# Optimization experiments

Measured on AMD Instinct MI355X. Metric: run time of the kernel, lower is better.

The kernel has to match this reference:

```python
import jax, jax.numpy as jnp
import numpy as np

EPS = 1e-5  # torch nn.LayerNorm default


def layer_norm(x, g, b):
    mu = jnp.mean(x, axis=-1, keepdims=True)
    var = jnp.mean(jnp.square(x - mu), axis=-1, keepdims=True)
    return (x - mu) * jax.lax.rsqrt(var + EPS) * g + b


def run_dir(g_ih_seq, w_hh, g_hh, b_hh, g_ho, b_ho, reverse):
    """Run one LayerNormLSTMCell direction over precomputed LN(x @ W_ih^T).
    g_ih_seq: [S, B, 4H]. Returns final hidden [B, H]."""
    S, B, G = g_ih_seq.shape
    H = G // 4

    def step(carry, gih_t):
        h, c = carry
        gates = gih_t + layer_norm(h @ w_hh.T, g_hh, b_hh)  # [B, 4H]
        i, f, o = jnp.split(jax.nn.sigmoid(gates[:, : 3 * H]), 3, axis=1)
        g = jnp.tanh(gates[:, 3 * H :])
        c = f * c + i * g
        h = o * jnp.tanh(layer_norm(c, g_ho, b_ho))
        return (h, c), None

    z = jnp.zeros((B, H), g_ih_seq.dtype)
    (hT, _), _ = jax.lax.scan(step, (z, z), g_ih_seq, reverse=reverse)
    return hT


def lnlstm(x, w_ih0, w_hh0, ln_ih0_g, ln_ih0_b, ln_hh0_g, ln_hh0_b, ln_ho0_g,
           ln_ho0_b, w_ih1, w_hh1, ln_ih1_g, ln_ih1_b, ln_hh1_g, ln_hh1_b,
           ln_ho1_g, ln_ho1_b):
    # x: [B, S, E] -> permute(1,0,2)
    x_seq = jnp.transpose(x, (1, 0, 2))  # [S, B, E]
    S, B, _ = x_seq.shape

    # ---- layer 0 (time-varying input) ----
    g0f = layer_norm(jnp.einsum('sbe,ge->sbg', x_seq, w_ih0[0]), ln_ih0_g[0], ln_ih0_b[0])
    hf = run_dir(g0f, w_hh0[0], ln_hh0_g[0], ln_hh0_b[0], ln_ho0_g[0], ln_ho0_b[0], False)
    g0b = layer_norm(jnp.einsum('sbe,ge->sbg', x_seq, w_ih0[1]), ln_ih0_g[1], ln_ih0_b[1])
    hb = run_dir(g0b, w_hh0[1], ln_hh0_g[1], ln_hh0_b[1], ln_ho0_g[1], ln_ho0_b[1], True)

    # Due to the `[[None]*N]*seq_len` aliasing bug in the original torch code,
    # the next layer's input is the SAME vector at every timestep:
    xc = jnp.concatenate([hf, hb], axis=1)  # [B, 2H]

    # ---- layer 1 (constant input; LN(x@W_ih^T) computed once, broadcast over time) ----
    g1f = layer_norm(xc @ w_ih1[0].T, ln_ih1_g[0], ln_ih1_b[0])
    hf1 = run_dir(jnp.broadcast_to(g1f, (S,) + g1f.shape), w_hh1[0],
                  ln_hh1_g[0], ln_hh1_b[0], ln_ho1_g[0], ln_ho1_b[0], False)
    g1b = layer_norm(xc @ w_ih1[1].T, ln_ih1_g[1], ln_ih1_b[1])
    hb1 = run_dir(jnp.broadcast_to(g1b, (S,) + g1b.shape), w_hh1[1],
                  ln_hh1_g[1], ln_hh1_b[1], ln_ho1_g[1], ln_ho1_b[1], True)

    # y = max over time of identical vectors == the vector itself
    return jnp.concatenate([hf1, hb1], axis=1)  # [B, 2H]


def setup_inputs() -> dict:
    key = jax.random.key(0)
    ks = jax.random.split(key, 20)
    B, S, E, H = 64, 48, 512, 512
    f = jnp.float32
    n = jax.random.normal
    u = jax.random.uniform
    return {
        'x': n(ks[0], (B, S, E), f),
        'text_length': jax.random.randint(ks[1], (B,), 1, S),
        'w_ih0': n(ks[2], (2, 4 * H, E), f) * 0.05,
        'w_hh0': n(ks[3], (2, 4 * H, H), f) * 0.05,
        'ln_ih0_g': u(ks[4], (2, 4 * H), f, 0.5, 1.5),
        'ln_ih0_b': n(ks[5], (2, 4 * H), f) * 0.02,
        'ln_hh0_g': u(ks[6], (2, 4 * H), f, 0.5, 1.5),
        'ln_hh0_b': n(ks[7], (2, 4 * H), f) * 0.02,
        'ln_ho0_g': u(ks[8], (2, H), f, 0.5, 1.5),
        'ln_ho0_b': n(ks[9], (2, H), f) * 0.02,
        'w_ih1': n(ks[10], (2, 4 * H, 2 * H), f) * 0.05,
        'w_hh1': n(ks[11], (2, 4 * H, H), f) * 0.05,
        'ln_ih1_g': u(ks[12], (2, 4 * H), f, 0.5, 1.5),
        'ln_ih1_b': n(ks[13], (2, 4 * H), f) * 0.02,
        'ln_hh1_g': u(ks[14], (2, 4 * H), f, 0.5, 1.5),
        'ln_hh1_b': n(ks[15], (2, 4 * H), f) * 0.02,
        'ln_ho1_g': u(ks[16], (2, H), f, 0.5, 1.5),
        'ln_ho1_b': n(ks[17], (2, H), f) * 0.02,
    }


def reference(x, text_length, w_ih0, w_hh0, ln_ih0_g, ln_ih0_b, ln_hh0_g,
              ln_hh0_b, ln_ho0_g, ln_ho0_b, w_ih1, w_hh1, ln_ih1_g, ln_ih1_b,
              ln_hh1_g, ln_hh1_b, ln_ho1_g, ln_ho1_b):
    # text_length is accepted but unused by the original forward
    return lnlstm(x, w_ih0, w_hh0, ln_ih0_g, ln_ih0_b, ln_hh0_g, ln_hh0_b,
                  ln_ho0_g, ln_ho0_b, w_ih1, w_hh1, ln_ih1_g, ln_ih1_b,
                  ln_hh1_g, ln_hh1_b, ln_ho1_g, ln_ho1_b)
```

## Files before the change

### kernel.cpp

```cpp
#include <hip/hip_runtime.h>
#include <math.h>

#define HH 512
#define BB 64
#define SS 48
#define EE 512
#define G4 2048
#define EPSF 1e-5f
#define AGENT __HIP_MEMORY_SCOPE_AGENT

__device__ __forceinline__ float aload(const float* p) {
  return __hip_atomic_load(p, __ATOMIC_RELAXED, AGENT);
}
__device__ __forceinline__ void astore(float* p, float v) {
  __hip_atomic_store(p, v, __ATOMIC_RELAXED, AGENT);
}

__device__ __forceinline__ float fsigmoid(float x) {
  float t = __builtin_amdgcn_exp2f(x * -1.44269504088896f);
  return __builtin_amdgcn_rcpf(1.f + t);
}
__device__ __forceinline__ float ftanh(float x) {
  x = fminf(fmaxf(x, -10.f), 10.f);
  float t = __builtin_amdgcn_exp2f(x * 2.88539008177793f);
  return (t - 1.f) * __builtin_amdgcn_rcpf(t + 1.f);
}

__device__ __forceinline__ void gsync(int* c, int target) {
  __builtin_amdgcn_s_waitcnt(0);
  __syncthreads();
  if (threadIdx.x == 0) {
    __hip_atomic_fetch_add(c, 1, __ATOMIC_RELEASE, AGENT);
    int spins = 0;
    while (__hip_atomic_load(c, __ATOMIC_RELAXED, AGENT) < target) {
      __builtin_amdgcn_s_sleep(2);
      if (++spins > (1 << 21)) break;
    }
    (void)__hip_atomic_load(c, __ATOMIC_ACQUIRE, AGENT);
  }
  __syncthreads();
}

__global__ __launch_bounds__(256)
void gemm_ih0(const float* __restrict__ x, const float* __restrict__ w_ih0,
              float* __restrict__ G0) {
  __shared__ float As[16][65];
  __shared__ float Bs[16][65];
  const int m0 = blockIdx.y * 64;
  const int d  = m0 / (BB * SS);
  const float* Wm = w_ih0 + (size_t)d * G4 * EE;
  const int bn = blockIdx.x * 64;
  const int tid = threadIdx.x;
  const int lrow = tid >> 2;
  const int lkk  = (tid & 3) << 2;
  const int tx = tid & 15;
  const int ty = tid >> 4;
  int m  = m0 + lrow;
  int r  = m - d * (BB * SS);
  int b  = r / SS;
  int tl = r - b * SS;
  int s  = d ? (SS - 1 - tl) : tl;
  const float* arow = x + ((size_t)b * SS + s) * EE;

  float acc[4][4] = {};
  for (int k0 = 0; k0 < EE; k0 += 16) {
    float4 av = *(const float4*)(arow + k0 + lkk);
    float4 bv = *(const float4*)(Wm + (size_t)(bn + lrow) * EE + k0 + lkk);
    As[lkk+0][lrow] = av.x; As[lkk+1][lrow] = av.y; As[lkk+2][lrow] = av.z; As[lkk+3][lrow] = av.w;
    Bs[lkk+0][lrow] = bv.x; Bs[lkk+1][lrow] = bv.y; Bs[lkk+2][lrow] = bv.z; Bs[lkk+3][lrow] = bv.w;
    __syncthreads();
    #pragma unroll
    for (int k = 0; k < 16; ++k) {
      float a[4], bbv[4];
      #pragma unroll
      for (int i = 0; i < 4; ++i) a[i] = As[k][ty*4+i];
      #pragma unroll
      for (int j = 0; j < 4; ++j) bbv[j] = Bs[k][tx*4+j];
      #pragma unroll
      for (int i = 0; i < 4; ++i)
        #pragma unroll
        for (int j = 0; j < 4; ++j) acc[i][j] += a[i]*bbv[j];
    }
    __syncthreads();
  }
  for (int i = 0; i < 4; ++i)
    for (int j = 0; j < 4; ++j)
      G0[(size_t)(m0 + ty*4 + i) * G4 + bn + tx*4 + j] = acc[i][j];
}

__global__ __launch_bounds__(256)
void ln_rows(float* __restrict__ X, const float* __restrict__ gamma,
             const float* __restrict__ beta, int rows_per_d) {
  __shared__ float red[8];
  const int row = blockIdx.x;
  const int d = row / rows_per_d;
  float* xr = X + (size_t)row * G4;
  const float* gg = gamma + (size_t)d * G4;
  const float* bb = beta  + (size_t)d * G4;
  float s = 0.f, q = 0.f;
  float v[8];
  #pragma unroll
  for (int it = 0; it < 8; ++it) {
    float xv = xr[threadIdx.x + it*256];
    v[it] = xv; s += xv; q += xv*xv;
  }
  #pragma unroll
  for (int off = 32; off > 0; off >>= 1) { s += __shfl_down(s, off); q += __shfl_down(q, off); }
  int lane = threadIdx.x & 63, wid = threadIdx.x >> 6;
  if (lane == 0) { red[wid] = s; red[4+wid] = q; }
  __syncthreads();
  float ts = red[0]+red[1]+red[2]+red[3];
  float tq = red[4]+red[5]+red[6]+red[7];
  float mu = ts * (1.f/G4);
  float rstd = rsqrtf(tq*(1.f/G4) - mu*mu + EPSF);
  #pragma unroll
  for (int it = 0; it < 8; ++it) {
    int jc = threadIdx.x + it*256;
    xr[jc] = (v[it]-mu)*rstd*gg[jc] + bb[jc];
  }
}

__global__ __launch_bounds__(1024, 4)
void persist7(const float* __restrict__ whh, const float* __restrict__ Gbuf,
              long g_row_stride, long g_t_stride,
              const float* __restrict__ lnhg, const float* __restrict__ lnhb,
              const float* __restrict__ lnog, const float* __restrict__ lnob,
              float* cbuf, float* obuf, float* Rpart, float* Cpart,
              int* flagsA, int* flagsB,
              float* fout, int nsteps,
              int mode1, const float* __restrict__ w_ih1,
              const float* __restrict__ xcb, float* g1pre,
              const float* __restrict__ ln_g1, const float* __restrict__ ln_b1,
              int* cnt_pre) {
  __shared__ float hlds[16][1024];
  __shared__ float part[16][8][64];
  __shared__ float redR[16][64];
  __shared__ float bcR[16][2];
  __shared__ float bcC[16][2];
  __shared__ float sred[32];

  const int bb = blockIdx.x;
  const int tid = threadIdx.x;

  if (mode1) {
    const int dp = bb & 1, nbp = bb >> 1;
    const int pb = tid >> 4, ns = tid & 15;
    const int col = nbp*16 + ns;
    const float* xrow = xcb + (size_t)pb * 1024;
    const float* wv_ = w_ih1 + ((size_t)dp*G4 + col) * 1024;
    float a = 0.f;
    for (int k = 0; k < 1024; k += 4) {
      float4 xv = *(const float4*)(xrow + k);
      float4 wv4 = *(const float4*)(wv_ + k);
      a += xv.x*wv4.x + xv.y*wv4.y + xv.z*wv4.z + xv.w*wv4.w;
    }
    astore(g1pre + ((size_t)dp*BB + pb) * G4 + col, a);
    gsync(cnt_pre + 0, 256);
    if (bb < 128) {
      const int ld = bb >> 6;
      float* xr = g1pre + (size_t)bb * G4;
      const float* gg = ln_g1 + (size_t)ld * G4;
      const float* be = ln_b1 + (size_t)ld * G4;
      float v0 = aload(xr + tid), v1 = aload(xr + tid + 1024);
      float s = v0 + v1, q = v0*v0 + v1*v1;
      #pragma unroll
      for (int off = 32; off > 0; off >>= 1) { s += __shfl_down(s, off); q += __shfl_down(q, off); }
      const int wv2 = tid >> 6;
      if ((tid & 63) == 0) { sred[wv2] = s; sred[16+wv2] = q; }
      __syncthreads();
      float ts = 0.f, tq = 0.f;
      #pragma unroll
      for (int i = 0; i < 16; ++i) { ts += sred[i]; tq += sred[16+i]; }
      float mu = ts * (1.f/G4);
      float rstd = rsqrtf(tq*(1.f/G4) - mu*mu + EPSF);
      astore(xr + tid,        (v0-mu)*rstd*gg[tid]      + be[tid]);
      astore(xr + tid + 1024, (v1-mu)*rstd*gg[tid+1024] + be[tid+1024]);
    }
    gsync(cnt_pre + 16, 256);
  }

  const int g  = bb & 7;
  const int d  = g >> 2;
  const int bq = g & 3;
  const int jb = bb >> 3;
  const int rowbase = d*BB + bq*16;
  const int ke = tid >> 6, nl = tid & 63;
  const int ncol = jb*16 + ((nl>>4) << 9) + (nl & 15);
  int* fA = flagsA + g*1024;
  int* fB = flagsB + g*1024;

  float wreg[32];
  {
    const float* wp = whh + ((size_t)d*G4 + ncol)*HH + (size_t)ke*32;
    #pragma unroll
    for (int i = 0; i < 32; ++i) wreg[i] = wp[i];
  }

  const int bl = tid >> 4, jl = tid & 15;
  const int rowc = rowbase + bl;
  const int jc = jb*16 + jl;
  const int scol = tid & 511, srh = tid >> 9;
  const float ogv = lnog[(size_t)d*HH + scol];
  const float obv = lnob[(size_t)d*HH + scol];
  const int row16 = tid >> 5, j32 = tid & 31;
  const int inv_g = (g_t_stride == 0);

  float hg0=0,hg1=0,hg2=0,hg3=0, hb0=0,hb1=0,hb2=0,hb3=0;
  float cg0=0,cg1=0,cg2=0,cg3=0;
  if (tid < 256) {
    const float* lnhg_d = lnhg + (size_t)d*G4;
    const float* lnhb_d = lnhb + (size_t)d*G4;
    hg0 = lnhg_d[jc];        hb0 = lnhb_d[jc];
    hg1 = lnhg_d[HH+jc];     hb1 = lnhb_d[HH+jc];
    hg2 = lnhg_d[2*HH+jc];   hb2 = lnhb_d[2*HH+jc];
    hg3 = lnhg_d[3*HH+jc];   hb3 = lnhb_d[3*HH+jc];
    if (inv_g) {
      const float* gr = Gbuf + (size_t)rowc * g_row_stride;
      cg0 = gr[jc]; cg1 = gr[HH+jc]; cg2 = gr[2*HH+jc]; cg3 = gr[3*HH+jc];
    }
  }
  float creg = 0.f;

  for (int t = 0; t < nsteps; ++t) {
    float cv[8], ovv[8];
    #pragma unroll
    for (int i = 0; i < 8; ++i) {
      int row = i*2 + srh;
      cv[i]  = aload(cbuf + (size_t)(rowbase + row)*512 + scol);
      ovv[i] = aload(obuf + (size_t)(rowbase + row)*512 + scol);
    }
    if (tid < 512) {
      float s = aload(Cpart + ((size_t)(rowbase+row16)*32 + j32)*2 + 0);
      float q = aload(Cpart + ((size_t)(rowbase+row16)*32 + j32)*2 + 1);
      #pragma unroll
      for (int off = 16; off > 0; off >>= 1) { s += __shfl_down(s, off, 32); q += __shfl_down(q, off, 32); }
      if (j32 == 0) {
        float mu = s * (1.f/HH);
        bcC[row16][0] = mu;
        bcC[row16][1] = rsqrtf(q*(1.f/HH) - mu*mu + EPSF);
      }
    }
    __syncthreads();
    #pragma unroll
    for (int i = 0; i < 8; ++i) {
      int row = i*2 + srh;
      hlds[row][scol] = ovv[i] * ftanh((cv[i] - bcC[row][0]) * bcC[row][1] * ogv + obv);
    }
    __syncthreads();

    #pragma unroll
    for (int half = 0; half < 2; ++half) {
      #pragma unroll
      for (int b = 0; b < 8; ++b) {
        const float* hp = &hlds[half*8 + b][ke*32];
        float acc = 0.f;
        #pragma unroll
        for (int i4 = 0; i4 < 8; ++i4) {
          float4 h4 = *(const float4*)(hp + 4*i4);
          acc += h4.x*wreg[4*i4+0] + h4.y*wreg[4*i4+1]
               + h4.z*wreg[4*i4+2] + h4.w*wreg[4*i4+3];
        }
        part[ke][b][nl] = acc;
      }
      __syncthreads();
      if (tid < 512) {
        int b = tid >> 6, n2 = tid & 63;
        float r = 0.f;
        #pragma unroll
        for (int k16 = 0; k16 < 16; ++k16) r += part[k16][b][n2];
        redR[half*8 + b][n2] = r;
      }
      __syncthreads();
    }
    if (tid < 512) {
      float v1 = redR[row16][j32], v2 = redR[row16][j32+32];
      float s = v1 + v2, q = v1*v1 + v2*v2;
      #pragma unroll
      for (int off = 16; off > 0; off >>= 1) { s += __shfl_down(s, off, 32); q += __shfl_down(q, off, 32); }
      if (j32 == 0) {
        astore(Rpart + ((size_t)(rowbase+row16)*32 + jb)*2 + 0, s);
        astore(Rpart + ((size_t)(rowbase+row16)*32 + jb)*2 + 1, q);
      }
    }
    float pg0 = cg0, pg1 = cg1, pg2 = cg2, pg3 = cg3;
    if (tid < 256 && !inv_g) {
      const float* gr = Gbuf + (size_t)rowc * g_row_stride + (size_t)t * g_t_stride;
      pg0 = gr[jc]; pg1 = gr[HH+jc]; pg2 = gr[2*HH+jc]; pg3 = gr[3*HH+jc];
    }
    __syncthreads();
    if (tid == 0) __hip_atomic_store(fA + jb*32, t + 1, __ATOMIC_RELAXED, AGENT);
    if (tid < 32) {
      int spins = 0;
      for (;;) {
        int v = __hip_atomic_load(fA + tid*32, __ATOMIC_RELAXED, AGENT);
        #pragma unroll
        for (int off = 16; off > 0; off >>= 1) v = min(v, __shfl_down(v, off, 32));
        v = __shfl(v, 0, 32);
        if (v >= t + 1) break;
        __builtin_amdgcn_s_sleep(1);
        if (++spins > (1 << 22)) break;
      }
    }
    __syncthreads();

    if (tid < 512) {
      float s = aload(Rpart + ((size_t)(rowbase+row16)*32 + j32)*2 + 0);
      float q = aload(Rpart + ((size_t)(rowbase+row16)*32 + j32)*2 + 1);
      #pragma unroll
      for (int off = 16; off > 0; off >>= 1) { s += __shfl_down(s, off, 32); q += __shfl_down(q, off, 32); }
      if (j32 == 0) {
        float mu = s * (1.f/G4);
        bcR[row16][0] = mu;
        bcR[row16][1] = rsqrtf(q*(1.f/G4) - mu*mu + EPSF);
      }
    }
    __syncthreads();

    if (tid < 256) {
      float mu = bcR[bl][0], rstd = bcR[bl][1];
      float gi = pg0 + (redR[bl][jl]    - mu)*rstd*hg0 + hb0;
      float gf = pg1 + (redR[bl][16+jl] - mu)*rstd*hg1 + hb1;
      float go = pg2 + (redR[bl][32+jl] - mu)*rstd*hg2 + hb2;
      float gt = pg3 + (redR[bl][48+jl] - mu)*rstd*hg3 + hb3;
      float iv = fsigmoid(gi), fv = fsigmoid(gf);
      float ov = fsigmoid(go), gv = ftanh(gt);
      creg = fv*creg + iv*gv;
      float cs = creg, cq = creg*creg;
      #pragma unroll
      for (int off = 8; off > 0; off >>= 1) { cs += __shfl_down(cs, off, 16); cq += __shfl_down(cq, off, 16); }
      if (jl == 0) {
        astore(Cpart + ((size_t)rowc*32 + jb)*2 + 0, cs);
        astore(Cpart + ((size_t)rowc*32 + jb)*2 + 1, cq);
      }
      astore(cbuf + (size_t)rowc*512 + jc, creg);
      astore(obuf + (size_t)rowc*512 + jc, ov);
    }
    __syncthreads();
    if (tid == 0) __hip_atomic_store(fB + jb*32, t + 1, __ATOMIC_RELAXED, AGENT);
    if (tid < 32) {
      int spins = 0;
      for (;;) {
        int v = __hip_atomic_load(fB + tid*32, __ATOMIC_RELAXED, AGENT);
        #pragma unroll
        for (int off = 16; off > 0; off >>= 1) v = min(v, __shfl_down(v, off, 32));
        v = __shfl(v, 0, 32);
        if (v >= t + 1) break;
        __builtin_amdgcn_s_sleep(1);
        if (++spins > (1 << 22)) break;
      }
    }
    __syncthreads();
  }

  {
    float cv[8], ovv[8];
    #pragma unroll
    for (int i = 0; i < 8; ++i) {
      int row = i*2 + srh;
      cv[i]  = aload(cbuf + (size_t)(rowbase + row)*512 + scol);
      ovv[i] = aload(obuf + (size_t)(rowbase + row)*512 + scol);
    }
    if (tid < 512) {
      float s = aload(Cpart + ((size_t)(rowbase+row16)*32 + j32)*2 + 0);
      float q = aload(Cpart + ((size_t)(rowbase+row16)*32 + j32)*2 + 1);
      #pragma unroll
      for (int off = 16; off > 0; off >>= 1) { s += __shfl_down(s, off, 32); q += __shfl_down(q, off, 32); }
      if (j32 == 0) {
        float mu = s * (1.f/HH);
        bcC[row16][0] = mu;
        bcC[row16][1] = rsqrtf(q*(1.f/HH) - mu*mu + EPSF);
      }
    }
    __syncthreads();
    if (jb == 0) {
      #pragma unroll
      for (int i = 0; i < 8; ++i) {
        int row = i*2 + srh;
        float h = ovv[i] * ftanh((cv[i] - bcC[row][0]) * bcC[row][1] * ogv + obv);
        fout[(size_t)(bq*16 + row) * 1024 + (size_t)d*512 + scol] = h;
      }
    }
  }
}

extern "C" void kernel_launch(void* const* d_in, const int* in_sizes, int n_in,
                              void* d_out, int out_size, void* d_ws, size_t ws_size,
                              hipStream_t stream) {
  const float* x        = (const float*)d_in[0];
  const float* w_ih0    = (const float*)d_in[2];
  const float* w_hh0    = (const float*)d_in[3];
  const float* ln_ih0_g = (const float*)d_in[4];
  const float* ln_ih0_b = (const float*)d_in[5];
  const float* ln_hh0_g = (const float*)d_in[6];
  const float* ln_hh0_b = (const float*)d_in[7];
  const float* ln_ho0_g = (const float*)d_in[8];
  const float* ln_ho0_b = (const float*)d_in[9];
  const float* w_ih1    = (const float*)d_in[10];
  const float* w_hh1    = (const float*)d_in[11];
  const float* ln_ih1_g = (const float*)d_in[12];
  const float* ln_ih1_b = (const float*)d_in[13];
  const float* ln_hh1_g = (const float*)d_in[14];
  const float* ln_hh1_b = (const float*)d_in[15];
  const float* ln_ho1_g = (const float*)d_in[16];
  const float* ln_ho1_b = (const float*)d_in[17];
  float* out = (float*)d_out;

  float* G0    = (float*)d_ws;
  float* g1pre = G0 + (size_t)2*BB*SS*G4;
  float* xcb   = g1pre + (size_t)2*BB*G4;
  float* Rpart = xcb + (size_t)BB*1024;
  float* Cpart = Rpart + (size_t)128*32*2;
  float* cbuf  = Cpart + (size_t)128*32*2;
  float* obuf  = cbuf + (size_t)128*512;
  int*   ints  = (int*)(obuf + (size_t)128*512);
  int*   fA0     = ints;
  int*   fB0     = ints + 8192;
  int*   fA1     = ints + 16384;
  int*   fB1     = ints + 24576;
  int*   cnt_pre = ints + 32768;

  hipMemsetAsync(Cpart, 0, ((size_t)128*32*2 + 2*(size_t)128*512)*sizeof(float)
                           + 32832*sizeof(int), stream);

  hipLaunchKernelGGL(gemm_ih0, dim3(G4/64, (2*BB*SS)/64), dim3(256), 0, stream,
      x, w_ih0, G0);
  hipLaunchKernelGGL(ln_rows, dim3(2*BB*SS), dim3(256), 0, stream,
      G0, ln_ih0_g, ln_ih0_b, BB*SS);

  hipLaunchKernelGGL(persist7, dim3(256), dim3(1024), 0, stream,
      w_hh0, G0, (long)SS*G4, (long)G4,
      ln_hh0_g, ln_hh0_b, ln_ho0_g, ln_ho0_b,
      cbuf, obuf, Rpart, Cpart, fA0, fB0, xcb, SS,
      0, (const float*)nullptr, (const float*)nullptr, (float*)nullptr,
      (const float*)nullptr, (const float*)nullptr, (int*)nullptr);

  hipMemsetAsync(Cpart, 0, ((size_t)128*32*2 + 2*(size_t)128*512)*sizeof(float), stream);

  hipLaunchKernelGGL(persist7, dim3(256), dim3(1024), 0, stream,
      w_hh1, g1pre, (long)G4, 0L,
      ln_hh1_g, ln_hh1_b, ln_ho1_g, ln_ho1_b,
      cbuf, obuf, Rpart, Cpart, fA1, fB1, out, SS,
      1, w_ih1, xcb, g1pre, ln_ih1_g, ln_ih1_b, cnt_pre);
}
```

Measured before the change: 1.752 ms.

## Compute recurrent LayerNorm statistics from h via precomputed Gram matrix W^T W

```diff
diff --git a/kernel.cpp b/kernel.cpp
--- a/kernel.cpp
+++ b/kernel.cpp
@@ -89,6 +89,54 @@
 }
 
 __global__ __launch_bounds__(256)
+void wtw(const float* __restrict__ w0, const float* __restrict__ w1,
+         float* __restrict__ M0, float* __restrict__ M1,
+         float* __restrict__ ws0, float* __restrict__ ws1) {
+  __shared__ float As[16][65];
+  __shared__ float Bs[16][65];
+  const int z = blockIdx.z;
+  const float* W = (z < 2 ? w0 : w1) + (size_t)(z & 1) * G4 * HH;
+  float* Mout  = (z < 2 ? M0 : M1) + (size_t)(z & 1) * HH * HH;
+  float* wsout = (z < 2 ? ws0 : ws1) + (size_t)(z & 1) * HH;
+  const int k1b = blockIdx.y * 64;
+  const int k2b = blockIdx.x * 64;
+  const int tid = threadIdx.x;
+  const int jj = tid >> 4;
+  const int c4 = (tid & 15) << 2;
+  const int tx = tid & 15, ty = tid >> 4;
+
+  float acc[4][4] = {};
+  float wsacc[4] = {0.f, 0.f, 0.f, 0.f};
+  for (int j0 = 0; j0 < G4; j0 += 16) {
+    float4 av = *(const float4*)(W + (size_t)(j0 + jj)*HH + k1b + c4);
+    float4 bv = *(const float4*)(W + (size_t)(j0 + jj)*HH + k2b + c4);
+    As[jj][c4+0]=av.x; As[jj][c4+1]=av.y; As[jj][c4+2]=av.z; As[jj][c4+3]=av.w;
+    Bs[jj][c4+0]=bv.x; Bs[jj][c4+1]=bv.y; Bs[jj][c4+2]=bv.z; Bs[jj][c4+3]=bv.w;
+    __syncthreads();
+    #pragma unroll
+    for (int k = 0; k < 16; ++k) {
+      float a[4], b[4];
+      #pragma unroll
+      for (int i = 0; i < 4; ++i) a[i] = As[k][ty*4+i];
+      #pragma unroll
+      for (int j = 0; j < 4; ++j) b[j] = Bs[k][tx*4+j];
+      #pragma unroll
+      for (int i = 0; i < 4; ++i) {
+        wsacc[i] += a[i];
+        #pragma unroll
+        for (int j = 0; j < 4; ++j) acc[i][j] += a[i]*b[j];
+      }
+    }
+    __syncthreads();
+  }
+  for (int i = 0; i < 4; ++i)
+    for (int j = 0; j < 4; ++j)
+      Mout[(size_t)(k1b + ty*4 + i)*HH + k2b + tx*4 + j] = acc[i][j];
+  if (blockIdx.x == 0 && tx == 0)
+    for (int i = 0; i < 4; ++i) wsout[k1b + ty*4 + i] = wsacc[i];
+}
+
+__global__ __launch_bounds__(256)
 void ln_rows(float* __restrict__ X, const float* __restrict__ gamma,
              const float* __restrict__ beta, int rows_per_d) {
   __shared__ float red[8];
@@ -131,13 +179,16 @@
               int mode1, const float* __restrict__ w_ih1,
               const float* __restrict__ xcb, float* g1pre,
               const float* __restrict__ ln_g1, const float* __restrict__ ln_b1,
-              int* cnt_pre) {
+              int* cnt_pre,
+              const float* __restrict__ Mmat, const float* __restrict__ wsum) {
   __shared__ float hlds[16][1024];
   __shared__ float part[16][8][64];
+  __shared__ float Mlds[16][512];
   __shared__ float redR[16][64];
   __shared__ float bcR[16][2];
   __shared__ float bcC[16][2];
   __shared__ float sred[32];
+  __shared__ float wsls[16];
 
   const int bb = blockIdx.x;
   const int tid = threadIdx.x;
@@ -196,6 +247,14 @@
     for (int i = 0; i < 32; ++i) wreg[i] = wp[i];
   }
 
+  {
+    float* mf = &Mlds[0][0];
+    const float* msrc = Mmat + (size_t)d*HH*HH + (size_t)(jb*16)*HH;
+    #pragma unroll
+    for (int u = 0; u < 8; ++u) mf[u*1024 + tid] = msrc[(size_t)u*1024 + tid];
+    if (tid < 16) wsls[tid] = wsum[(size_t)d*HH + jb*16 + tid];
+  }
+
   const int bl = tid >> 4, jl = tid & 15;
   const int rowc = rowbase + bl;
   const int jc = jb*16 + jl;
@@ -204,6 +263,7 @@
   const float obv = lnob[(size_t)d*HH + scol];
   const int row16 = tid >> 5, j32 = tid & 31;
   const int inv_g = (g_t_stride == 0);
+  const int kbase = jb*16;
 
   float hg0=0,hg1=0,hg2=0,hg3=0, hb0=0,hb1=0,hb2=0,hb3=0;
   float cg0=0,cg1=0,cg2=0,cg3=0;
@@ -248,6 +308,34 @@
     }
     __syncthreads();
 
+    if (tid < 512) {
+      const int r = row16;
+      float hreg[16];
+      #pragma unroll
+      for (int k1 = 0; k1 < 16; ++k1) hreg[k1] = hlds[r][kbase + k1];
+      float t_s = 0.f;
+      #pragma unroll
+      for (int k1 = 0; k1 < 16; ++k1) t_s += hreg[k1] * wsls[k1];
+      float t_q = 0.f;
+      #pragma unroll
+      for (int it = 0; it < 16; ++it) {
+        int k2 = j32 + 32*it;
+        float h2 = hlds[r][k2];
+        float dcol = 0.f;
+        #pragma unroll
+        for (int k1 = 0; k1 < 16; ++k1) dcol += Mlds[k1][k2] * hreg[k1];
+        t_q += h2 * dcol;
+      }
+      #pragma unroll
+      for (int off = 16; off > 0; off >>= 1) t_q += __shfl_down(t_q, off, 32);
+      if (j32 == 0) {
+        astore(Rpart + ((size_t)(rowbase+r)*32 + jb)*2 + 0, t_s);
+        astore(Rpart + ((size_t)(rowbase+r)*32 + jb)*2 + 1, t_q);
+      }
+    }
+    __syncthreads();
+    if (tid == 0) __hip_atomic_store(fA + jb*32, t + 1, __ATOMIC_RELAXED, AGENT);
+
     #pragma unroll
     for (int half = 0; half < 2; ++half) {
       #pragma unroll
@@ -272,23 +360,11 @@
       }
       __syncthreads();
     }
-    if (tid < 512) {
-      float v1 = redR[row16][j32], v2 = redR[row16][j32+32];
-      float s = v1 + v2, q = v1*v1 + v2*v2;
-      #pragma unroll
-      for (int off = 16; off > 0; off >>= 1) { s += __shfl_down(s, off, 32); q += __shfl_down(q, off, 32); }
-      if (j32 == 0) {
-        astore(Rpart + ((size_t)(rowbase+row16)*32 + jb)*2 + 0, s);
-        astore(Rpart + ((size_t)(rowbase+row16)*32 + jb)*2 + 1, q);
-      }
-    }
     float pg0 = cg0, pg1 = cg1, pg2 = cg2, pg3 = cg3;
     if (tid < 256 && !inv_g) {
       const float* gr = Gbuf + (size_t)rowc * g_row_stride + (size_t)t * g_t_stride;
       pg0 = gr[jc]; pg1 = gr[HH+jc]; pg2 = gr[2*HH+jc]; pg3 = gr[3*HH+jc];
     }
-    __syncthreads();
-    if (tid == 0) __hip_atomic_store(fA + jb*32, t + 1, __ATOMIC_RELAXED, AGENT);
     if (tid < 32) {
       int spins = 0;
       for (;;) {
@@ -409,7 +485,11 @@
   float* g1pre = G0 + (size_t)2*BB*SS*G4;
   float* xcb   = g1pre + (size_t)2*BB*G4;
   float* Rpart = xcb + (size_t)BB*1024;
-  float* Cpart = Rpart + (size_t)128*32*2;
+  float* M0    = Rpart + (size_t)128*32*2;
+  float* M1    = M0 + (size_t)2*HH*HH;
+  float* ws0   = M1 + (size_t)2*HH*HH;
+  float* ws1   = ws0 + (size_t)2*HH;
+  float* Cpart = ws1 + (size_t)2*HH;
   float* cbuf  = Cpart + (size_t)128*32*2;
   float* obuf  = cbuf + (size_t)128*512;
   int*   ints  = (int*)(obuf + (size_t)128*512);
@@ -422,6 +502,9 @@
   hipMemsetAsync(Cpart, 0, ((size_t)128*32*2 + 2*(size_t)128*512)*sizeof(float)
                            + 32832*sizeof(int), stream);
 
+  hipLaunchKernelGGL(wtw, dim3(8, 8, 4), dim3(256), 0, stream,
+      w_hh0, w_hh1, M0, M1, ws0, ws1);
+
   hipLaunchKernelGGL(gemm_ih0, dim3(G4/64, (2*BB*SS)/64), dim3(256), 0, stream,
       x, w_ih0, G0);
   hipLaunchKernelGGL(ln_rows, dim3(2*BB*SS), dim3(256), 0, stream,
@@ -432,7 +515,8 @@
       ln_hh0_g, ln_hh0_b, ln_ho0_g, ln_ho0_b,
       cbuf, obuf, Rpart, Cpart, fA0, fB0, xcb, SS,
       0, (const float*)nullptr, (const float*)nullptr, (float*)nullptr,
-      (const float*)nullptr, (const float*)nullptr, (int*)nullptr);
+      (const float*)nullptr, (const float*)nullptr, (int*)nullptr,
+      M0, ws0);
 
   hipMemsetAsync(Cpart, 0, ((size_t)128*32*2 + 2*(size_t)128*512)*sizeof(float), stream);
 
@@ -440,5 +524,6 @@
       w_hh1, g1pre, (long)G4, 0L,
       ln_hh1_g, ln_hh1_b, ln_ho1_g, ln_ho1_b,
       cbuf, obuf, Rpart, Cpart, fA1, fB1, out, SS,
-      1, w_ih1, xcb, g1pre, ln_ih1_g, ln_ih1_b, cnt_pre);
-}
+      1, w_ih1, xcb, g1pre, ln_ih1_g, ln_ih1_b, cnt_pre,
+      M1, ws1);
+}
```

New measurement: 2.395 ms. 1.37x slower.

## Replace flag barrier A with timestamped 16-byte partial-stat records polled directly

Applied to the files above, without the earlier changes.

```diff
diff --git a/kernel.cpp b/kernel.cpp
--- a/kernel.cpp
+++ b/kernel.cpp
@@ -9,11 +9,25 @@
 #define EPSF 1e-5f
 #define AGENT __HIP_MEMORY_SCOPE_AGENT
 
+typedef __attribute__((ext_vector_type(4))) float f32x4;
+
 __device__ __forceinline__ float aload(const float* p) {
   return __hip_atomic_load(p, __ATOMIC_RELAXED, AGENT);
 }
 __device__ __forceinline__ void astore(float* p, float v) {
   __hip_atomic_store(p, v, __ATOMIC_RELAXED, AGENT);
+}
+
+__device__ __forceinline__ f32x4 ld4c(const float* p) {
+  f32x4 v;
+  asm volatile("global_load_dwordx4 %0, %1, off sc0 sc1\n\ts_waitcnt vmcnt(0)"
+               : "=&v"(v) : "v"(p) : "memory");
+  return v;
+}
+__device__ __forceinline__ void st4c(float* p, float a, float b, float tg) {
+  f32x4 v; v.x = a; v.y = b; v.z = tg; v.w = 0.f;
+  asm volatile("global_store_dwordx4 %0, %1, off sc0 sc1"
+               :: "v"(p), "v"(v) : "memory");
 }
 
 __device__ __forceinline__ float fsigmoid(float x) {
@@ -125,8 +139,8 @@
               long g_row_stride, long g_t_stride,
               const float* __restrict__ lnhg, const float* __restrict__ lnhb,
               const float* __restrict__ lnog, const float* __restrict__ lnob,
-              float* cbuf, float* obuf, float* Rpart, float* Cpart,
-              int* flagsA, int* flagsB,
+              float* cbuf, float* obuf, float* Rp4, float* Cpart,
+              int* flagsB,
               float* fout, int nsteps,
               int mode1, const float* __restrict__ w_ih1,
               const float* __restrict__ xcb, float* g1pre,
@@ -186,8 +200,7 @@
   const int rowbase = d*BB + bq*16;
   const int ke = tid >> 6, nl = tid & 63;
   const int ncol = jb*16 + ((nl>>4) << 9) + (nl & 15);
-  int* fA = flagsA + g*1024;
-  int* fB = flagsB + g*1024;
+  int* fB = flagsB + g*32;
 
   float wreg[32];
   {
@@ -204,6 +217,9 @@
   const float obv = lnob[(size_t)d*HH + scol];
   const int row16 = tid >> 5, j32 = tid & 31;
   const int inv_g = (g_t_stride == 0);
+
+  float* rpub4 = Rp4 + ((size_t)((rowbase + row16)*32 + jb) << 2);
+  const float* rpp4 = Rp4 + ((size_t)((rowbase + row16)*32 + j32) << 2);
 
   float hg0=0,hg1=0,hg2=0,hg3=0, hb0=0,hb1=0,hb2=0,hb3=0;
   float cg0=0,cg1=0,cg2=0,cg3=0;
@@ -222,6 +238,7 @@
   float creg = 0.f;
 
   for (int t = 0; t < nsteps; ++t) {
+    const float ft1 = (float)(t + 1);
     float cv[8], ovv[8];
     #pragma unroll
     for (int i = 0; i < 8; ++i) {
@@ -277,35 +294,22 @@
       float s = v1 + v2, q = v1*v1 + v2*v2;
       #pragma unroll
       for (int off = 16; off > 0; off >>= 1) { s += __shfl_down(s, off, 32); q += __shfl_down(q, off, 32); }
-      if (j32 == 0) {
-        astore(Rpart + ((size_t)(rowbase+row16)*32 + jb)*2 + 0, s);
-        astore(Rpart + ((size_t)(rowbase+row16)*32 + jb)*2 + 1, q);
-      }
+      if (j32 == 0) st4c(rpub4, s, q, ft1);
     }
     float pg0 = cg0, pg1 = cg1, pg2 = cg2, pg3 = cg3;
     if (tid < 256 && !inv_g) {
       const float* gr = Gbuf + (size_t)rowc * g_row_stride + (size_t)t * g_t_stride;
       pg0 = gr[jc]; pg1 = gr[HH+jc]; pg2 = gr[2*HH+jc]; pg3 = gr[3*HH+jc];
     }
-    __syncthreads();
-    if (tid == 0) __hip_atomic_store(fA + jb*32, t + 1, __ATOMIC_RELAXED, AGENT);
-    if (tid < 32) {
+    if (tid < 512) {
+      f32x4 rp = ld4c(rpp4);
       int spins = 0;
-      for (;;) {
-        int v = __hip_atomic_load(fA + tid*32, __ATOMIC_RELAXED, AGENT);
-        #pragma unroll
-        for (int off = 16; off > 0; off >>= 1) v = min(v, __shfl_down(v, off, 32));
-        v = __shfl(v, 0, 32);
-        if (v >= t + 1) break;
+      while (rp.z < ft1) {
         __builtin_amdgcn_s_sleep(1);
-        if (++spins > (1 << 22)) break;
-      }
-    }
-    __syncthreads();
-
-    if (tid < 512) {
-      float s = aload(Rpart + ((size_t)(rowbase+row16)*32 + j32)*2 + 0);
-      float q = aload(Rpart + ((size_t)(rowbase+row16)*32 + j32)*2 + 1);
+        rp = ld4c(rpp4);
+        if (++spins > (1 << 20)) break;
+      }
+      float s = rp.x, q = rp.y;
       #pragma unroll
       for (int off = 16; off > 0; off >>= 1) { s += __shfl_down(s, off, 32); q += __shfl_down(q, off, 32); }
       if (j32 == 0) {
@@ -336,11 +340,11 @@
       astore(obuf + (size_t)rowc*512 + jc, ov);
     }
     __syncthreads();
-    if (tid == 0) __hip_atomic_store(fB + jb*32, t + 1, __ATOMIC_RELAXED, AGENT);
+    if (tid == 0) __hip_atomic_store(fB + jb, t + 1, __ATOMIC_RELAXED, AGENT);
     if (tid < 32) {
       int spins = 0;
       for (;;) {
-        int v = __hip_atomic_load(fB + tid*32, __ATOMIC_RELAXED, AGENT);
+        int v = __hip_atomic_load(fB + tid, __ATOMIC_RELAXED, AGENT);
         #pragma unroll
         for (int off = 16; off > 0; off >>= 1) v = min(v, __shfl_down(v, off, 32));
         v = __shfl(v, 0, 32);
@@ -408,19 +412,18 @@
   float* G0    = (float*)d_ws;
   float* g1pre = G0 + (size_t)2*BB*SS*G4;
   float* xcb   = g1pre + (size_t)2*BB*G4;
-  float* Rpart = xcb + (size_t)BB*1024;
-  float* Cpart = Rpart + (size_t)128*32*2;
+  float* Rp4   = xcb + (size_t)BB*1024;
+  float* Cpart = Rp4 + (size_t)128*32*4;
   float* cbuf  = Cpart + (size_t)128*32*2;
   float* obuf  = cbuf + (size_t)128*512;
   int*   ints  = (int*)(obuf + (size_t)128*512);
-  int*   fA0     = ints;
-  int*   fB0     = ints + 8192;
-  int*   fA1     = ints + 16384;
-  int*   fB1     = ints + 24576;
-  int*   cnt_pre = ints + 32768;
-
-  hipMemsetAsync(Cpart, 0, ((size_t)128*32*2 + 2*(size_t)128*512)*sizeof(float)
-                           + 32832*sizeof(int), stream);
+  int*   fB0     = ints;
+  int*   fB1     = ints + 256;
+  int*   cnt_pre = ints + 512;
+
+  const size_t zr_floats = (size_t)128*32*4 + (size_t)128*32*2 + 2*(size_t)128*512;
+
+  hipMemsetAsync(Rp4, 0, zr_floats*sizeof(float) + 576*sizeof(int), stream);
 
   hipLaunchKernelGGL(gemm_ih0, dim3(G4/64, (2*BB*SS)/64), dim3(256), 0, stream,
       x, w_ih0, G0);
@@ -430,15 +433,15 @@
   hipLaunchKernelGGL(persist7, dim3(256), dim3(1024), 0, stream,
       w_hh0, G0, (long)SS*G4, (long)G4,
       ln_hh0_g, ln_hh0_b, ln_ho0_g, ln_ho0_b,
-      cbuf, obuf, Rpart, Cpart, fA0, fB0, xcb, SS,
+      cbuf, obuf, Rp4, Cpart, fB0, xcb, SS,
       0, (const float*)nullptr, (const float*)nullptr, (float*)nullptr,
       (const float*)nullptr, (const float*)nullptr, (int*)nullptr);
 
-  hipMemsetAsync(Cpart, 0, ((size_t)128*32*2 + 2*(size_t)128*512)*sizeof(float), stream);
+  hipMemsetAsync(Rp4, 0, zr_floats*sizeof(float), stream);
 
   hipLaunchKernelGGL(persist7, dim3(256), dim3(1024), 0, stream,
       w_hh1, g1pre, (long)G4, 0L,
       ln_hh1_g, ln_hh1_b, ln_ho1_g, ln_ho1_b,
-      cbuf, obuf, Rpart, Cpart, fA1, fB1, out, SS,
+      cbuf, obuf, Rp4, Cpart, fB1, out, SS,
       1, w_ih1, xcb, g1pre, ln_ih1_g, ln_ih1_b, cnt_pre);
 }
```

New measurement: 1.963 ms. 12.1% more time.

## Split per-step recurrence into two half-batch pipelines with separate grid flags

Applied to the files above, without the earlier changes.

```diff
diff --git a/kernel.cpp b/kernel.cpp
--- a/kernel.cpp
+++ b/kernel.cpp
@@ -39,6 +39,21 @@
     (void)__hip_atomic_load(c, __ATOMIC_ACQUIRE, AGENT);
   }
   __syncthreads();
+}
+
+__device__ __forceinline__ void flagpoll(const int* f, int t1, int tid) {
+  if (tid < 32) {
+    int spins = 0;
+    for (;;) {
+      int v = __hip_atomic_load(f + tid*32, __ATOMIC_RELAXED, AGENT);
+      #pragma unroll
+      for (int off = 16; off > 0; off >>= 1) v = min(v, __shfl_down(v, off, 32));
+      v = __shfl(v, 0, 32);
+      if (v >= t1) break;
+      __builtin_amdgcn_s_sleep(1);
+      if (++spins > (1 << 22)) break;
+    }
+  }
 }
 
 __global__ __launch_bounds__(256)
@@ -121,7 +136,7 @@
 }
 
 __global__ __launch_bounds__(1024, 4)
-void persist7(const float* __restrict__ whh, const float* __restrict__ Gbuf,
+void persistP(const float* __restrict__ whh, const float* __restrict__ Gbuf,
               long g_row_stride, long g_t_stride,
               const float* __restrict__ lnhg, const float* __restrict__ lnhb,
               const float* __restrict__ lnog, const float* __restrict__ lnob,
@@ -132,7 +147,7 @@
               const float* __restrict__ xcb, float* g1pre,
               const float* __restrict__ ln_g1, const float* __restrict__ ln_b1,
               int* cnt_pre) {
-  __shared__ float hlds[16][1024];
+  __shared__ float hlds[16][520];
   __shared__ float part[16][8][64];
   __shared__ float redR[16][64];
   __shared__ float bcR[16][2];
@@ -145,16 +160,16 @@
   if (mode1) {
     const int dp = bb & 1, nbp = bb >> 1;
     const int pb = tid >> 4, ns = tid & 15;
-    const int col = nbp*16 + ns;
+    const int col1 = nbp*16 + ns;
     const float* xrow = xcb + (size_t)pb * 1024;
-    const float* wv_ = w_ih1 + ((size_t)dp*G4 + col) * 1024;
+    const float* wv_ = w_ih1 + ((size_t)dp*G4 + col1) * 1024;
     float a = 0.f;
     for (int k = 0; k < 1024; k += 4) {
       float4 xv = *(const float4*)(xrow + k);
       float4 wv4 = *(const float4*)(wv_ + k);
       a += xv.x*wv4.x + xv.y*wv4.y + xv.z*wv4.z + xv.w*wv4.w;
     }
-    astore(g1pre + ((size_t)dp*BB + pb) * G4 + col, a);
+    astore(g1pre + ((size_t)dp*BB + pb) * G4 + col1, a);
     gsync(cnt_pre + 0, 256);
     if (bb < 128) {
       const int ld = bb >> 6;
@@ -186,8 +201,10 @@
   const int rowbase = d*BB + bq*16;
   const int ke = tid >> 6, nl = tid & 63;
   const int ncol = jb*16 + ((nl>>4) << 9) + (nl & 15);
-  int* fA = flagsA + g*1024;
-  int* fB = flagsB + g*1024;
+  int* fA0 = flagsA + g*1024;
+  int* fA1 = flagsA + 8192 + g*1024;
+  int* fB0 = flagsB + g*1024;
+  int* fB1 = flagsB + 8192 + g*1024;
 
   float wreg[32];
   {
@@ -196,18 +213,20 @@
     for (int i = 0; i < 32; ++i) wreg[i] = wp[i];
   }
 
-  const int bl = tid >> 4, jl = tid & 15;
-  const int rowc = rowbase + bl;
+  const int bl = tid >> 4;
+  const int jl = tid & 15;
   const int jc = jb*16 + jl;
   const int scol = tid & 511, srh = tid >> 9;
   const float ogv = lnog[(size_t)d*HH + scol];
   const float obv = lnob[(size_t)d*HH + scol];
-  const int row16 = tid >> 5, j32 = tid & 31;
+  const int row8 = (tid >> 5) & 7, j32 = tid & 31;
   const int inv_g = (g_t_stride == 0);
+  const int rowcA = rowbase + bl;
+  const int rowcB = rowbase + 8 + bl;
 
   float hg0=0,hg1=0,hg2=0,hg3=0, hb0=0,hb1=0,hb2=0,hb3=0;
-  float cg0=0,cg1=0,cg2=0,cg3=0;
-  if (tid < 256) {
+  float cgA0=0,cgA1=0,cgA2=0,cgA3=0, cgB0=0,cgB1=0,cgB2=0,cgB3=0;
+  if (tid < 128) {
     const float* lnhg_d = lnhg + (size_t)d*G4;
     const float* lnhb_d = lnhb + (size_t)d*G4;
     hg0 = lnhg_d[jc];        hb0 = lnhb_d[jc];
@@ -215,170 +234,213 @@
     hg2 = lnhg_d[2*HH+jc];   hb2 = lnhb_d[2*HH+jc];
     hg3 = lnhg_d[3*HH+jc];   hb3 = lnhb_d[3*HH+jc];
     if (inv_g) {
-      const float* gr = Gbuf + (size_t)rowc * g_row_stride;
-      cg0 = gr[jc]; cg1 = gr[HH+jc]; cg2 = gr[2*HH+jc]; cg3 = gr[3*HH+jc];
-    }
-  }
-  float creg = 0.f;
+      const float* ga = Gbuf + (size_t)rowcA * g_row_stride;
+      const float* gb = Gbuf + (size_t)rowcB * g_row_stride;
+      cgA0 = ga[jc]; cgA1 = ga[HH+jc]; cgA2 = ga[2*HH+jc]; cgA3 = ga[3*HH+jc];
+      cgB0 = gb[jc]; cgB1 = gb[HH+jc]; cgB2 = gb[2*HH+jc]; cgB3 = gb[3*HH+jc];
+    }
+  }
+  {
+    float* hz = &hlds[0][0];
+    for (int u = tid; u < 16*520; u += 1024) hz[u] = 0.f;
+  }
+  __syncthreads();
+
+  float cregA = 0.f, cregB = 0.f;
 
   for (int t = 0; t < nsteps; ++t) {
-    float cv[8], ovv[8];
-    #pragma unroll
-    for (int i = 0; i < 8; ++i) {
-      int row = i*2 + srh;
-      cv[i]  = aload(cbuf + (size_t)(rowbase + row)*512 + scol);
-      ovv[i] = aload(obuf + (size_t)(rowbase + row)*512 + scol);
-    }
+    #pragma unroll
+    for (int b = 0; b < 8; ++b) {
+      const float* hp = &hlds[b][ke*32];
+      float acc = 0.f;
+      #pragma unroll
+      for (int i4 = 0; i4 < 8; ++i4) {
+        float4 h4 = *(const float4*)(hp + 4*i4);
+        acc += h4.x*wreg[4*i4+0] + h4.y*wreg[4*i4+1]
+             + h4.z*wreg[4*i4+2] + h4.w*wreg[4*i4+3];
+      }
+      part[ke][b][nl] = acc;
+    }
+    __syncthreads();
     if (tid < 512) {
-      float s = aload(Cpart + ((size_t)(rowbase+row16)*32 + j32)*2 + 0);
-      float q = aload(Cpart + ((size_t)(rowbase+row16)*32 + j32)*2 + 1);
+      int b = tid >> 6, n2 = tid & 63;
+      float r = 0.f;
+      #pragma unroll
+      for (int k16 = 0; k16 < 16; ++k16) r += part[k16][b][n2];
+      redR[b][n2] = r;
+      float s = r, q = r*r;
+      #pragma unroll
+      for (int off = 32; off > 0; off >>= 1) { s += __shfl_down(s, off); q += __shfl_down(q, off); }
+      if (n2 == 0) {
+        astore(Rpart + ((size_t)(rowbase + b)*32 + jb)*2 + 0, s);
+        astore(Rpart + ((size_t)(rowbase + b)*32 + jb)*2 + 1, q);
+      }
+    }
+    __syncthreads();
+    if (tid == 0) __hip_atomic_store(fA0 + jb*32, t + 1, __ATOMIC_RELAXED, AGENT);
+
+    #pragma unroll
+    for (int b = 0; b < 8; ++b) {
+      const float* hp = &hlds[8 + b][ke*32];
+      float acc = 0.f;
+      #pragma unroll
+      for (int i4 = 0; i4 < 8; ++i4) {
+        float4 h4 = *(const float4*)(hp + 4*i4);
+        acc += h4.x*wreg[4*i4+0] + h4.y*wreg[4*i4+1]
+             + h4.z*wreg[4*i4+2] + h4.w*wreg[4*i4+3];
+      }
+      part[ke][b][nl] = acc;
+    }
+    __syncthreads();
+    if (tid < 512) {
+      int b = tid >> 6, n2 = tid & 63;
+      float r = 0.f;
+      #pragma unroll
+      for (int k16 = 0; k16 < 16; ++k16) r += part[k16][b][n2];
+      redR[8 + b][n2] = r;
+      float s = r, q = r*r;
+      #pragma unroll
+      for (int off = 32; off > 0; off >>= 1) { s += __shfl_down(s, off); q += __shfl_down(q, off); }
+      if (n2 == 0) {
+        astore(Rpart + ((size_t)(rowbase + 8 + b)*32 + jb)*2 + 0, s);
+        astore(Rpart + ((size_t)(rowbase + 8 + b)*32 + jb)*2 + 1, q);
+      }
+    }
+    __syncthreads();
+    if (tid == 0) __hip_atomic_store(fA1 + jb*32, t + 1, __ATOMIC_RELAXED, AGENT);
+
+    float pA0=cgA0,pA1=cgA1,pA2=cgA2,pA3=cgA3;
+    float pB0=cgB0,pB1=cgB1,pB2=cgB2,pB3=cgB3;
+    if (tid < 128 && !inv_g) {
+      const float* ga = Gbuf + (size_t)rowcA * g_row_stride + (size_t)t * g_t_stride;
+      const float* gb = Gbuf + (size_t)rowcB * g_row_stride + (size_t)t * g_t_stride;
+      pA0 = ga[jc]; pA1 = ga[HH+jc]; pA2 = ga[2*HH+jc]; pA3 = ga[3*HH+jc];
+      pB0 = gb[jc]; pB1 = gb[HH+jc]; pB2 = gb[2*HH+jc]; pB3 = gb[3*HH+jc];
+    }
+
+    flagpoll(fA0, t + 1, tid);
+    __syncthreads();
+    if (tid < 256) {
+      float s = aload(Rpart + ((size_t)(rowbase+row8)*32 + j32)*2 + 0);
+      float q = aload(Rpart + ((size_t)(rowbase+row8)*32 + j32)*2 + 1);
+      #pragma unroll
+      for (int off = 16; off > 0; off >>= 1) { s += __shfl_down(s, off, 32); q += __shfl_down(q, off, 32); }
+      if (j32 == 0) {
+        float mu = s * (1.f/G4);
+        bcR[row8][0] = mu;
+        bcR[row8][1] = rsqrtf(q*(1.f/G4) - mu*mu + EPSF);
+      }
+    }
+    __syncthreads();
+    if (tid < 128) {
+      float mu = bcR[bl][0], rstd = bcR[bl][1];
+      float gi = pA0 + (redR[bl][jl]    - mu)*rstd*hg0 + hb0;
+      float gf = pA1 + (redR[bl][16+jl] - mu)*rstd*hg1 + hb1;
+      float go = pA2 + (redR[bl][32+jl] - mu)*rstd*hg2 + hb2;
+      float gt = pA3 + (redR[bl][48+jl] - mu)*rstd*hg3 + hb3;
+      float iv = fsigmoid(gi), fv = fsigmoid(gf);
+      float ov = fsigmoid(go), gv = ftanh(gt);
+      cregA = fv*cregA + iv*gv;
+      float cs = cregA, cq = cregA*cregA;
+      #pragma unroll
+      for (int off = 8; off > 0; off >>= 1) { cs += __shfl_down(cs, off, 16); cq += __shfl_down(cq, off, 16); }
+      if (jl == 0) {
+        astore(Cpart + ((size_t)rowcA*32 + jb)*2 + 0, cs);
+        astore(Cpart + ((size_t)rowcA*32 + jb)*2 + 1, cq);
+      }
+      astore(cbuf + (size_t)rowcA*512 + jc, cregA);
+      astore(obuf + (size_t)rowcA*512 + jc, ov);
+    }
+    __syncthreads();
+    if (tid == 0) __hip_atomic_store(fB0 + jb*32, t + 1, __ATOMIC_RELAXED, AGENT);
+
+    flagpoll(fA1, t + 1, tid);
+    __syncthreads();
+    if (tid < 256) {
+      float s = aload(Rpart + ((size_t)(rowbase+8+row8)*32 + j32)*2 + 0);
+      float q = aload(Rpart + ((size_t)(rowbase+8+row8)*32 + j32)*2 + 1);
+      #pragma unroll
+      for (int off = 16; off > 0; off >>= 1) { s += __shfl_down(s, off, 32); q += __shfl_down(q, off, 32); }
+      if (j32 == 0) {
+        float mu = s * (1.f/G4);
+        bcR[8+row8][0] = mu;
+        bcR[8+row8][1] = rsqrtf(q*(1.f/G4) - mu*mu + EPSF);
+      }
+    }
+    __syncthreads();
+    if (tid < 128) {
+      float mu = bcR[8+bl][0], rstd = bcR[8+bl][1];
+      float gi = pB0 + (redR[8+bl][jl]    - mu)*rstd*hg0 + hb0;
+      float gf = pB1 + (redR[8+bl][16+jl] - mu)*rstd*hg1 + hb1;
+      float go = pB2 + (redR[8+bl][32+jl] - mu)*rstd*hg2 + hb2;
+      float gt = pB3 + (redR[8+bl][48+jl] - mu)*rstd*hg3 + hb3;
+      float iv = fsigmoid(gi), fv = fsigmoid(gf);
+      float ov = fsigmoid(go), gv = ftanh(gt);
+      cregB = fv*cregB + iv*gv;
+      float cs = cregB, cq = cregB*cregB;
+      #pragma unroll
+      for (int off = 8; off > 0; off >>= 1) { cs += __shfl_down(cs, off, 16); cq += __shfl_down(cq, off, 16); }
+      if (jl == 0) {
+        astore(Cpart + ((size_t)rowcB*32 + jb)*2 + 0, cs);
+        astore(Cpart + ((size_t)rowcB*32 + jb)*2 + 1, cq);
+      }
+      astore(cbuf + (size_t)rowcB*512 + jc, cregB);
+      astore(obuf + (size_t)rowcB*512 + jc, ov);
+    }
+    __syncthreads();
+    if (tid == 0) __hip_atomic_store(fB1 + jb*32, t + 1, __ATOMIC_RELAXED, AGENT);
+
+    flagpoll(fB0, t + 1, tid);
+    __syncthreads();
+    if (tid < 256) {
+      float s = aload(Cpart + ((size_t)(rowbase+row8)*32 + j32)*2 + 0);
+      float q = aload(Cpart + ((size_t)(rowbase+row8)*32 + j32)*2 + 1);
       #pragma unroll
       for (int off = 16; off > 0; off >>= 1) { s += __shfl_down(s, off, 32); q += __shfl_down(q, off, 32); }
       if (j32 == 0) {
         float mu = s * (1.f/HH);
-        bcC[row16][0] = mu;
-        bcC[row16][1] = rsqrtf(q*(1.f/HH) - mu*mu + EPSF);
-      }
-    }
-    __syncthreads();
-    #pragma unroll
-    for (int i = 0; i < 8; ++i) {
+        bcC[row8][0] = mu;
+        bcC[row8][1] = rsqrtf(q*(1.f/HH) - mu*mu + EPSF);
+      }
+    }
+    __syncthreads();
+    #pragma unroll
+    for (int i = 0; i < 4; ++i) {
       int row = i*2 + srh;
-      hlds[row][scol] = ovv[i] * ftanh((cv[i] - bcC[row][0]) * bcC[row][1] * ogv + obv);
-    }
-    __syncthreads();
-
-    #pragma unroll
-    for (int half = 0; half < 2; ++half) {
-      #pragma unroll
-      for (int b = 0; b < 8; ++b) {
-        const float* hp = &hlds[half*8 + b][ke*32];
-        float acc = 0.f;
-        #pragma unroll
-        for (int i4 = 0; i4 < 8; ++i4) {
-          float4 h4 = *(const float4*)(hp + 4*i4);
-          acc += h4.x*wreg[4*i4+0] + h4.y*wreg[4*i4+1]
-               + h4.z*wreg[4*i4+2] + h4.w*wreg[4*i4+3];
-        }
-        part[ke][b][nl] = acc;
-      }
-      __syncthreads();
-      if (tid < 512) {
-        int b = tid >> 6, n2 = tid & 63;
-        float r = 0.f;
-        #pragma unroll
-        for (int k16 = 0; k16 < 16; ++k16) r += part[k16][b][n2];
-        redR[half*8 + b][n2] = r;
-      }
-      __syncthreads();
-    }
-    if (tid < 512) {
-      float v1 = redR[row16][j32], v2 = redR[row16][j32+32];
-      float s = v1 + v2, q = v1*v1 + v2*v2;
-      #pragma unroll
-      for (int off = 16; off > 0; off >>= 1) { s += __shfl_down(s, off, 32); q += __shfl_down(q, off, 32); }
-      if (j32 == 0) {
-        astore(Rpart + ((size_t)(rowbase+row16)*32 + jb)*2 + 0, s);
-        astore(Rpart + ((size_t)(rowbase+row16)*32 + jb)*2 + 1, q);
-      }
-    }
-    float pg0 = cg0, pg1 = cg1, pg2 = cg2, pg3 = cg3;
-    if (tid < 256 && !inv_g) {
-      const float* gr = Gbuf + (size_t)rowc * g_row_stride + (size_t)t * g_t_stride;
-      pg0 = gr[jc]; pg1 = gr[HH+jc]; pg2 = gr[2*HH+jc]; pg3 = gr[3*HH+jc];
-    }
-    __syncthreads();
-    if (tid == 0) __hip_atomic_store(fA + jb*32, t + 1, __ATOMIC_RELAXED, AGENT);
-    if (tid < 32) {
-      int spins = 0;
-      for (;;) {
-        int v = __hip_atomic_load(fA + tid*32, __ATOMIC_RELAXED, AGENT);
-        #pragma unroll
-        for (int off = 16; off > 0; off >>= 1) v = min(v, __shfl_down(v, off, 32));
-        v = __shfl(v, 0, 32);
-        if (v >= t + 1) break;
-        __builtin_amdgcn_s_sleep(1);
-        if (++spins > (1 << 22)) break;
-      }
-    }
-    __syncthreads();
-
-    if (tid < 512) {
-      float s = aload(Rpart + ((size_t)(rowbase+row16)*32 + j32)*2 + 0);
-      float q = aload(Rpart + ((size_t)(rowbase+row16)*32 + j32)*2 + 1);
-      #pragma unroll
-      for (int off = 16; off > 0; off >>= 1) { s += __shfl_down(s, off, 32); q += __shfl_down(q, off, 32); }
-      if (j32 == 0) {
-        float mu = s * (1.f/G4);
-        bcR[row16][0] = mu;
-        bcR[row16][1] = rsqrtf(q*(1.f/G4) - mu*mu + EPSF);
-      }
-    }
-    __syncthreads();
-
+      float c = aload(cbuf + (size_t)(rowbase + row)*512 + scol);
+      float o = aload(obuf + (size_t)(rowbase + row)*512 + scol);
+      hlds[row][scol] = o * ftanh((c - bcC[row][0]) * bcC[row][1] * ogv + obv);
+    }
+
+    flagpoll(fB1, t + 1, tid);
+    __syncthreads();
     if (tid < 256) {
-      float mu = bcR[bl][0], rstd = bcR[bl][1];
-      float gi = pg0 + (redR[bl][jl]    - mu)*rstd*hg0 + hb0;
-      float gf = pg1 + (redR[bl][16+jl] - mu)*rstd*hg1 + hb1;
-      float go = pg2 + (redR[bl][32+jl] - mu)*rstd*hg2 + hb2;
-      float gt = pg3 + (redR[bl][48+jl] - mu)*rstd*hg3 + hb3;
-      float iv = fsigmoid(gi), fv = fsigmoid(gf);
-      float ov = fsigmoid(go), gv = ftanh(gt);
-      creg = fv*creg + iv*gv;
-      float cs = creg, cq = creg*creg;
-      #pragma unroll
-      for (int off = 8; off > 0; off >>= 1) { cs += __shfl_down(cs, off, 16); cq += __shfl_down(cq, off, 16); }
-      if (jl == 0) {
-        astore(Cpart + ((size_t)rowc*32 + jb)*2 + 0, cs);
-        astore(Cpart + ((size_t)rowc*32 + jb)*2 + 1, cq);
-      }
-      astore(cbuf + (size_t)rowc*512 + jc, creg);
-      astore(obuf + (size_t)rowc*512 + jc, ov);
-    }
-    __syncthreads();
-    if (tid == 0) __hip_atomic_store(fB + jb*32, t + 1, __ATOMIC_RELAXED, AGENT);
-    if (tid < 32) {
-      int spins = 0;
-      for (;;) {
-        int v = __hip_atomic_load(fB + tid*32, __ATOMIC_RELAXED, AGENT);
-        #pragma unroll
-        for (int off = 16; off > 0; off >>= 1) v = min(v, __shfl_down(v, off, 32));
-        v = __shfl(v, 0, 32);
-        if (v >= t + 1) break;
-        __builtin_amdgcn_s_sleep(1);
-        if (++spins > (1 << 22)) break;
-      }
-    }
-    __syncthreads();
-  }
-
-  {
-    float cv[8], ovv[8];
-    #pragma unroll
-    for (int i = 0; i < 8; ++i) {
-      int row = i*2 + srh;
-      cv[i]  = aload(cbuf + (size_t)(rowbase + row)*512 + scol);
-      ovv[i] = aload(obuf + (size_t)(rowbase + row)*512 + scol);
-    }
-    if (tid < 512) {
-      float s = aload(Cpart + ((size_t)(rowbase+row16)*32 + j32)*2 + 0);
-      float q = aload(Cpart + ((size_t)(rowbase+row16)*32 + j32)*2 + 1);
+      float s = aload(Cpart + ((size_t)(rowbase+8+row8)*32 + j32)*2 + 0);
+      float q = aload(Cpart + ((size_t)(rowbase+8+row8)*32 + j32)*2 + 1);
       #pragma unroll
       for (int off = 16; off > 0; off >>= 1) { s += __shfl_down(s, off, 32); q += __shfl_down(q, off, 32); }
       if (j32 == 0) {
         float mu = s * (1.f/HH);
-        bcC[row16][0] = mu;
-        bcC[row16][1] = rsqrtf(q*(1.f/HH) - mu*mu + EPSF);
-      }
-    }
-    __syncthreads();
-    if (jb == 0) {
-      #pragma unroll
-      for (int i = 0; i < 8; ++i) {
-        int row = i*2 + srh;
-        float h = ovv[i] * ftanh((cv[i] - bcC[row][0]) * bcC[row][1] * ogv + obv);
-        fout[(size_t)(bq*16 + row) * 1024 + (size_t)d*512 + scol] = h;
-      }
+        bcC[8+row8][0] = mu;
+        bcC[8+row8][1] = rsqrtf(q*(1.f/HH) - mu*mu + EPSF);
+      }
+    }
+    __syncthreads();
+    #pragma unroll
+    for (int i = 0; i < 4; ++i) {
+      int row = 8 + i*2 + srh;
+      float c = aload(cbuf + (size_t)(rowbase + row)*512 + scol);
+      float o = aload(obuf + (size_t)(rowbase + row)*512 + scol);
+      hlds[row][scol] = o * ftanh((c - bcC[row][0]) * bcC[row][1] * ogv + obv);
+    }
+    __syncthreads();
+  }
+
+  if (jb == 0) {
+    #pragma unroll
+    for (int i = 0; i < 8; ++i) {
+      int row = i*2 + srh;
+      fout[(size_t)(bq*16 + row) * 1024 + (size_t)d*512 + scol] = hlds[row][scol];
     }
   }
 }
@@ -413,32 +475,30 @@
   float* cbuf  = Cpart + (size_t)128*32*2;
   float* obuf  = cbuf + (size_t)128*512;
   int*   ints  = (int*)(obuf + (size_t)128*512);
-  int*   fA0     = ints;
-  int*   fB0     = ints + 8192;
-  int*   fA1     = ints + 16384;
-  int*   fB1     = ints + 24576;
-  int*   cnt_pre = ints + 32768;
+  int*   fA_l0   = ints;
+  int*   fB_l0   = ints + 16384;
+  int*   fA_l1   = ints + 32768;
+  int*   fB_l1   = ints + 49152;
+  int*   cnt_pre = ints + 65536;
 
   hipMemsetAsync(Cpart, 0, ((size_t)128*32*2 + 2*(size_t)128*512)*sizeof(float)
-                           + 32832*sizeof(int), stream);
+                           + 65600*sizeof(int), stream);
 
   hipLaunchKernelGGL(gemm_ih0, dim3(G4/64, (2*BB*SS)/64), dim3(256), 0, stream,
       x, w_ih0, G0);
   hipLaunchKernelGGL(ln_rows, dim3(2*BB*SS), dim3(256), 0, stream,
       G0, ln_ih0_g, ln_ih0_b, BB*SS);
 
-  hipLaunchKernelGGL(persist7, dim3(256), dim3(1024), 0, stream,
+  hipLaunchKernelGGL(persistP, dim3(256), dim3(1024), 0, stream,
       w_hh0, G0, (long)SS*G4, (long)G4,
       ln_hh0_g, ln_hh0_b, ln_ho0_g, ln_ho0_b,
-      cbuf, obuf, Rpart, Cpart, fA0, fB0, xcb, SS,
+      cbuf, obuf, Rpart, Cpart, fA_l0, fB_l0, xcb, SS,
       0, (const float*)nullptr, (const float*)nullptr, (float*)nullptr,
       (const float*)nullptr, (const float*)nullptr, (int*)nullptr);
 
-  hipMemsetAsync(Cpart, 0, ((size_t)128*32*2 + 2*(size_t)128*512)*sizeof(float), stream);
-
-  hipLaunchKernelGGL(persist7, dim3(256), dim3(1024), 0, stream,
+  hipLaunchKernelGGL(persistP, dim3(256), dim3(1024), 0, stream,
       w_hh1, g1pre, (long)G4, 0L,
       ln_hh1_g, ln_hh1_b, ln_ho1_g, ln_ho1_b,
-      cbuf, obuf, Rpart, Cpart, fA1, fB1, out, SS,
+      cbuf, obuf, Rpart, Cpart, fA_l1, fB_l1, out, SS,
       1, w_ih1, xcb, g1pre, ln_ih1_g, ln_ih1_b, cnt_pre);
 }
```

After: 2.089 ms. 1.19x slower.
